# Performance work log

Measured on AMD Instinct MI355X. Metric: run time of the kernel, lower is better.

Reference implementation:

```python
import jax, jax.numpy as jnp
import numpy as np

SIGMA = 0.1
B = 1.0
SPATIAL_WEIGHT = 0.5
EPS = 1e-5


def setup_inputs() -> dict:
    key = jax.random.key(0)
    k1, k2 = jax.random.split(key)
    N, C, H, W = 2, 256, 64, 64
    I_features = jax.random.normal(k1, (N, C, H, W), dtype=jnp.float32)
    T_features = jax.random.normal(k2, (N, C, H, W), dtype=jnp.float32)
    return {"I_features": I_features, "T_features": T_features}


def _calc_cx(raw):
    # raw: [N, P_T, H, W]; min + exp-softmax over the target-patch axis (axis=1)
    mn = jnp.min(raw, axis=1, keepdims=True)
    rel = raw / (mn + EPS)
    w = jnp.exp((B - rel) / SIGMA)
    return w / jnp.sum(w, axis=1, keepdims=True)


def reference(I_features, T_features):
    N, C, H, W = I_features.shape
    P = H * W

    # ---- spatial branch: L2 distances on a normalized meshgrid (C=2) ----
    rows = jnp.arange(H, dtype=jnp.float32) / (H + 1)
    cols = jnp.arange(W, dtype=jnp.float32) / (W + 1)
    grid = jnp.stack(jnp.meshgrid(rows, cols, indexing="ij"))  # [2, H, W]
    g = grid.reshape(2, P)                                      # [2, P]
    sq = jnp.sum(g * g, axis=0)                                 # [P]
    d = sq[:, None] + sq[None, :] - 2.0 * (g.T @ g)             # [P_I, P_T]
    d = jnp.clip(d, 0.0)
    raw_sp = d.T.reshape(1, P, H, W)  # [1, P_T, H, W]; identical per sample
    cx_sp = _calc_cx(raw_sp)

    # ---- feature branch: cosine similarity via centered, L2-normed feats ----
    meanT = jnp.mean(T_features, axis=(0, 2, 3), keepdims=True)
    Ic = I_features - meanT
    Tc = T_features - meanT
    In = Ic / jnp.linalg.norm(Ic, axis=1, keepdims=True)
    Tn = Tc / jnp.linalg.norm(Tc, axis=1, keepdims=True)
    Iv = In.reshape(N, C, P)
    Tv = Tn.reshape(N, C, P)
    dot = jnp.einsum("ncq,ncp->nqp", Tv, Iv)  # [N, P_T, P_I]
    raw_feat = ((1.0 - dot) / 2.0).reshape(N, P, H, W)
    cx_feat = _calc_cx(raw_feat)

    # ---- combine, max over I positions, mean over T patches, -log, mean ----
    cx = (1.0 - SPATIAL_WEIGHT) * cx_feat + SPATIAL_WEIGHT * cx_sp  # [N,P,H,W]
    m = jnp.max(cx, axis=(2, 3))  # [N, P]
    m = jnp.mean(m, axis=1)       # [N]
    return jnp.mean(-jnp.log(m))
```

## Files before the change

kernel.cpp:

```cpp
#include <hip/hip_runtime.h>
#include <math.h>

#define PP 4096
#define CC 256
#define NN 2
#define NSTEP 16

typedef __attribute__((ext_vector_type(4))) float f32x4;
typedef __attribute__((ext_vector_type(8))) int i32x8;
typedef __attribute__((ext_vector_type(2))) int i32x2;


__global__ __launch_bounds__(256) void mean_kernel(const float* __restrict__ T,
                                                   float* __restrict__ meanT,
                                                   float* __restrict__ loss_acc) {
    int c = blockIdx.x, tid = threadIdx.x;
    float s = 0.f;
    for (int n = 0; n < NN; n++) {
        const float4* Tc = (const float4*)&T[(size_t)(n * CC + c) * PP];
        for (int g = 0; g < 4; g++) {
            float4 v = Tc[tid + g * 256];
            s += (v.x + v.y) + (v.z + v.w);
        }
    }
    __shared__ float red[256];
    red[tid] = s; __syncthreads();
    for (int st = 128; st > 0; st >>= 1) {
        if (tid < st) red[tid] += red[tid + st];
        __syncthreads();
    }
    if (tid == 0) meanT[c] = red[0] * (1.0f / (NN * PP));
    if (blockIdx.x == 0 && tid < NN) loss_acc[tid] = 0.f;
}

__global__ __launch_bounds__(256) void normalize_kernel(const float* __restrict__ I,
                                                        const float* __restrict__ T,
                                                        const float* __restrict__ meanT,
                                                        char* __restrict__ InT,
                                                        char* __restrict__ TnT) {
    int pc = blockIdx.x * 32;
    int n = blockIdx.y;
    int which = blockIdx.z;
    const float* X = which ? T : I;
    char* Y = (which ? TnT : InT) + (size_t)n * PP * CC;

    __shared__ float tile[CC][36];
    __shared__ float red[32][32];
    __shared__ float invn[32];

    int tid = threadIdx.x;
    int pl4 = tid & 7, c0 = tid >> 3;
    float sq0 = 0.f, sq1 = 0.f, sq2 = 0.f, sq3 = 0.f;
    for (int c = c0; c < CC; c += 32) {
        float m = meanT[c];
        float4 v = *(const float4*)&X[(size_t)(n * CC + c) * PP + pc + pl4 * 4];
        v.x -= m; v.y -= m; v.z -= m; v.w -= m;
        *(float4*)&tile[c][pl4 * 4] = v;
        sq0 += v.x * v.x; sq1 += v.y * v.y; sq2 += v.z * v.z; sq3 += v.w * v.w;
    }
    red[c0][pl4 * 4 + 0] = sq0;
    red[c0][pl4 * 4 + 1] = sq1;
    red[c0][pl4 * 4 + 2] = sq2;
    red[c0][pl4 * 4 + 3] = sq3;
    __syncthreads();
    if (tid < 32) {
        float s = 0.f;
        for (int k = 0; k < 32; k++) s += red[k][tid];
        invn[tid] = 1.0f / sqrtf(s);
    }
    __syncthreads();
    for (int pass = 0; pass < 8; pass++) {
        int r = pass * 4 + (tid >> 6);
        int p = pc + r;
        int c4 = (tid & 63) * 4;
        float in = invn[r];
        float v0 = tile[c4 + 0][r] * in;
        float v1 = tile[c4 + 1][r] * in;
        float v2 = tile[c4 + 2][r] * in;
        float v3 = tile[c4 + 3][r] * in;
        int w = __builtin_amdgcn_cvt_pk_fp8_f32(v0, v1, 0, false);
        w = __builtin_amdgcn_cvt_pk_fp8_f32(v2, v3, w, true);
        size_t addr = (size_t)(p >> 4) * 4096 + (c4 >> 5) * 512 +
                      ((c4 >> 3) & 3) * 128 + (p & 15) * 8 + (c4 & 7);
        *(unsigned*)&Y[addr] = (unsigned)w;
    }
}

__global__ __launch_bounds__(1024) void cx_strip(const char* __restrict__ TnT,
                                                 const char* __restrict__ InT,
                                                 float* __restrict__ loss_acc) {
    const int strip = blockIdx.x;
    const int n = blockIdx.y;
    const int p0 = strip * 32;
    const char* __restrict__ Ab = TnT + (size_t)n * PP * CC;
    const char* __restrict__ Bb = InT + (size_t)n * PP * CC;

    __shared__ float redw[16][32];
    __shared__ float inv2s[32];
    __shared__ float dwl[32];

    const int tid = threadIdx.x;
    const int l = tid & 63, wv = tid >> 6;
    const int lm = l & 15, quad = l >> 4;

    union BU { i32x2 d[2][8]; i32x8 v[2][2]; } bf;
#pragma unroll
    for (int ct = 0; ct < 2; ct++)
#pragma unroll
        for (int g = 0; g < 8; g++)
            bf.d[ct][g] = *(const i32x2*)(Bb + (size_t)(strip * 2 + ct) * 4096 +
                                          g * 512 + l * 8);

    const char* Abase = Ab + (size_t)wv * 4096 + l * 8;
    union AU { i32x2 d[8]; i32x8 v[2]; };

    float amax[2] = {-3.4e38f, -3.4e38f};
    float hc[2] = {0.f, 0.f}, c0c[2] = {0.f, 0.f};
    float ss[2] = {0.f, 0.f};
    const int qdd0 = p0 >> 8, wdd0 = (p0 >> 4) & 15;
    const int qdd1 = (p0 + 16) >> 8, wdd1 = ((p0 + 16) >> 4) & 15;

#pragma unroll 1
    for (int pass = 0; pass < 2; pass++) {
        AU cur, nxt;
#pragma unroll
        for (int g = 0; g < 8; g++)
            cur.d[g] = *(const i32x2*)(Abase + g * 512);

#pragma unroll 2
        for (int qs = 0; qs < NSTEP; qs++) {
            if (qs < NSTEP - 1) {
#pragma unroll
                for (int g = 0; g < 8; g++)
                    nxt.d[g] = *(const i32x2*)(Abase +
                        (size_t)(qs + 1) * 65536 + g * 512);
            }

            f32x4 acc[2] = {};
#pragma unroll
            for (int kb = 0; kb < 2; kb++)
#pragma unroll
                for (int ct = 0; ct < 2; ct++)
                    acc[ct] = __builtin_amdgcn_mfma_scale_f32_16x16x128_f8f6f4(
                        cur.v[kb], bf.v[ct][kb], acc[ct],
                        0, 0,
                        0, 0x7f7f7f7f,
                        0, 0x7f7f7f7f);

            if (pass == 0) {
#pragma unroll
                for (int ct = 0; ct < 2; ct++)
#pragma unroll
                    for (int e = 0; e < 4; e++)
                        amax[ct] = fmaxf(amax[ct], acc[ct][e]);
            } else {
#pragma unroll
                for (int ct = 0; ct < 2; ct++) {
                    float s2 = 0.f;
#pragma unroll
                    for (int e = 0; e < 4; e++)
                        s2 += exp2f(fmaf(acc[ct][e], hc[ct], c0c[ct]));
                    ss[ct] += s2;
                }
                if (qs == qdd0 && wv == wdd0 && quad == (lm >> 2))
                    dwl[lm] = exp2f(fmaf(acc[0][lm & 3], hc[0], c0c[0]));
                if (qs == qdd1 && wv == wdd1 && quad == (lm >> 2))
                    dwl[16 + lm] = exp2f(fmaf(acc[1][lm & 3], hc[1], c0c[1]));
            }

            if (qs < NSTEP - 1) cur = nxt;
        }

        if (pass == 0) {
#pragma unroll
            for (int ct = 0; ct < 2; ct++) {
                amax[ct] = fmaxf(amax[ct], __shfl_xor(amax[ct], 16));
                amax[ct] = fmaxf(amax[ct], __shfl_xor(amax[ct], 32));
                if (quad == 0) redw[wv][ct * 16 + lm] = amax[ct];
            }
            __syncthreads();
            if (tid < 32) {
                float mx = redw[0][tid];
#pragma unroll
                for (int w2 = 1; w2 < 16; w2++) mx = fmaxf(mx, redw[w2][tid]);
                float mnv = (1.0f - mx) * 0.5f;
                inv2s[tid] = 14.4269504f / (mnv + 1e-5f);
            }
            __syncthreads();
            {
                float i20 = inv2s[lm], i21 = inv2s[16 + lm];
                hc[0] = i20 * 0.5f; c0c[0] = 14.4269504f - hc[0];
                hc[1] = i21 * 0.5f; c0c[1] = 14.4269504f - hc[1];
            }
        }
    }

#pragma unroll
    for (int ct = 0; ct < 2; ct++) {
        ss[ct] += __shfl_xor(ss[ct], 16);
        ss[ct] += __shfl_xor(ss[ct], 32);
        if (quad == 0) redw[wv][ct * 16 + lm] = ss[ct];
    }
    __syncthreads();
    if (tid < 32) {
        float s = 0.f;
#pragma unroll
        for (int w2 = 0; w2 < 16; w2++) s += redw[w2][tid];
        float part = dwl[tid] / s;
        part += __shfl_xor(part, 1);
        part += __shfl_xor(part, 2);
        part += __shfl_xor(part, 4);
        part += __shfl_xor(part, 8);
        part += __shfl_xor(part, 16);
        if (tid == 0) atomicAdd(&loss_acc[n], part);
    }
}

__global__ void finalize_kernel(const float* __restrict__ loss_acc,
                                float* __restrict__ out) {
    float m0 = 0.5f + 0.5f * (loss_acc[0] / (float)PP);
    float m1 = 0.5f + 0.5f * (loss_acc[1] / (float)PP);
    out[0] = 0.5f * (-logf(m0) - logf(m1));
}

extern "C" void kernel_launch(void* const* d_in, const int* in_sizes, int n_in,
                              void* d_out, int out_size, void* d_ws, size_t ws_size,
                              hipStream_t stream) {
    const float* I = (const float*)d_in[0];
    const float* T = (const float*)d_in[1];
    float* out = (float*)d_out;

    char* ws = (char*)d_ws;
    const size_t SZ_F8 = (size_t)NN * PP * CC;
    char* InT = ws;
    char* TnT = ws + SZ_F8;
    float* meanT = (float*)(ws + 2 * SZ_F8);
    float* loss_acc = (float*)(ws + 2 * SZ_F8 + 32768);

    mean_kernel<<<CC, 256, 0, stream>>>(T, meanT, loss_acc);
    normalize_kernel<<<dim3(PP / 32, NN, 2), 256, 0, stream>>>(I, T, meanT, InT, TnT);
    cx_strip<<<dim3(PP / 32, NN), 1024, 0, stream>>>(TnT, InT, loss_acc);
    finalize_kernel<<<1, 1, 0, stream>>>(loss_acc, out);
}
```

Measured before the change: 110.0 us.

## Cache dot products in fp16 registers to drop second MFMA pass; stage A via LDS

The two-pass loop that recomputed the full FP8 MFMA GEMM (max pass, then exp-sum pass) becomes a single pass that keeps every dot product in registers as packed fp16 and then applies the exp-softmax sum from that cache. A tiles are now double-buffered through LDS with global_load_lds and explicit vmcnt waits instead of direct register loads. This halves GEMM work and global A traffic per strip, at the cost of 32 extra VGPRs per lane, 128KB of LDS per block, and fp16 rounding of the dot values before the exp.

```diff
diff --git a/kernel.cpp b/kernel.cpp
--- a/kernel.cpp
+++ b/kernel.cpp
@@ -9,6 +9,13 @@
 typedef __attribute__((ext_vector_type(4))) float f32x4;
 typedef __attribute__((ext_vector_type(8))) int i32x8;
 typedef __attribute__((ext_vector_type(2))) int i32x2;
+typedef _Float16 f16x2 __attribute__((ext_vector_type(2)));
+
+__device__ __forceinline__ void gld_lds16(const char* g, char* l) {
+    __builtin_amdgcn_global_load_lds(
+        (const __attribute__((address_space(1))) unsigned int*)g,
+        (__attribute__((address_space(3))) unsigned int*)l, 16, 0, 0);
+}
 
 
 __global__ __launch_bounds__(256) void mean_kernel(const float* __restrict__ T,
@@ -95,6 +102,7 @@
     const char* __restrict__ Ab = TnT + (size_t)n * PP * CC;
     const char* __restrict__ Bb = InT + (size_t)n * PP * CC;
 
+    __shared__ __align__(16) char Aw[16][2][4096];
     __shared__ float redw[16][32];
     __shared__ float inv2s[32];
     __shared__ float dwl[32];
@@ -111,87 +119,107 @@
             bf.d[ct][g] = *(const i32x2*)(Bb + (size_t)(strip * 2 + ct) * 4096 +
                                           g * 512 + l * 8);
 
-    const char* Abase = Ab + (size_t)wv * 4096 + l * 8;
-    union AU { i32x2 d[8]; i32x8 v[2]; };
-
+#define STAGE_A(qs, b)                                                        \
+    {                                                                         \
+        const char* s_ = Ab + (size_t)((qs) * 16 + wv) * 4096 + l * 16;       \
+        char* d_ = &Aw[wv][b][0] + l * 16;                                    \
+        _Pragma("unroll")                                                     \
+        for (int g_ = 0; g_ < 4; g_++)                                        \
+            gld_lds16(s_ + g_ * 1024, d_ + g_ * 1024);                        \
+    }
+
+    f16x2 dots[NSTEP][4];
     float amax[2] = {-3.4e38f, -3.4e38f};
-    float hc[2] = {0.f, 0.f}, c0c[2] = {0.f, 0.f};
-    float ss[2] = {0.f, 0.f};
     const int qdd0 = p0 >> 8, wdd0 = (p0 >> 4) & 15;
     const int qdd1 = (p0 + 16) >> 8, wdd1 = ((p0 + 16) >> 4) & 15;
 
-#pragma unroll 1
-    for (int pass = 0; pass < 2; pass++) {
-        AU cur, nxt;
+    STAGE_A(0, 0);
+#pragma unroll
+    for (int qs = 0; qs < NSTEP; qs++) {
+        if (qs < NSTEP - 1) {
+            STAGE_A(qs + 1, (qs + 1) & 1);
+            asm volatile("s_waitcnt vmcnt(4)" ::: "memory");
+        } else {
+            asm volatile("s_waitcnt vmcnt(0)" ::: "memory");
+        }
+        __builtin_amdgcn_sched_barrier(0);
+
+        const char* Ac = &Aw[wv][qs & 1][0];
+        union AU { long l2[8]; i32x8 v[2]; } a;
 #pragma unroll
         for (int g = 0; g < 8; g++)
-            cur.d[g] = *(const i32x2*)(Abase + g * 512);
-
-#pragma unroll 2
-        for (int qs = 0; qs < NSTEP; qs++) {
-            if (qs < NSTEP - 1) {
-#pragma unroll
-                for (int g = 0; g < 8; g++)
-                    nxt.d[g] = *(const i32x2*)(Abase +
-                        (size_t)(qs + 1) * 65536 + g * 512);
+            a.l2[g] = *(const long*)&Ac[g * 512 + l * 8];
+
+        f32x4 acc[2] = {};
+#pragma unroll
+        for (int kb = 0; kb < 2; kb++)
+#pragma unroll
+            for (int ct = 0; ct < 2; ct++)
+                acc[ct] = __builtin_amdgcn_mfma_scale_f32_16x16x128_f8f6f4(
+                    a.v[kb], bf.v[ct][kb], acc[ct],
+                    0, 0,
+                    0, 0x7f7f7f7f,
+                    0, 0x7f7f7f7f);
+
+#pragma unroll
+        for (int ct = 0; ct < 2; ct++) {
+#pragma unroll
+            for (int eh = 0; eh < 2; eh++) {
+                f16x2 t;
+                t.x = (_Float16)acc[ct][2 * eh];
+                t.y = (_Float16)acc[ct][2 * eh + 1];
+                dots[qs][ct * 2 + eh] = t;
             }
-
-            f32x4 acc[2] = {};
-#pragma unroll
-            for (int kb = 0; kb < 2; kb++)
-#pragma unroll
-                for (int ct = 0; ct < 2; ct++)
-                    acc[ct] = __builtin_amdgcn_mfma_scale_f32_16x16x128_f8f6f4(
-                        cur.v[kb], bf.v[ct][kb], acc[ct],
-                        0, 0,
-                        0, 0x7f7f7f7f,
-                        0, 0x7f7f7f7f);
-
-            if (pass == 0) {
-#pragma unroll
-                for (int ct = 0; ct < 2; ct++)
-#pragma unroll
-                    for (int e = 0; e < 4; e++)
-                        amax[ct] = fmaxf(amax[ct], acc[ct][e]);
-            } else {
-#pragma unroll
-                for (int ct = 0; ct < 2; ct++) {
-                    float s2 = 0.f;
-#pragma unroll
-                    for (int e = 0; e < 4; e++)
-                        s2 += exp2f(fmaf(acc[ct][e], hc[ct], c0c[ct]));
-                    ss[ct] += s2;
-                }
-                if (qs == qdd0 && wv == wdd0 && quad == (lm >> 2))
-                    dwl[lm] = exp2f(fmaf(acc[0][lm & 3], hc[0], c0c[0]));
-                if (qs == qdd1 && wv == wdd1 && quad == (lm >> 2))
-                    dwl[16 + lm] = exp2f(fmaf(acc[1][lm & 3], hc[1], c0c[1]));
-            }
-
-            if (qs < NSTEP - 1) cur = nxt;
-        }
-
-        if (pass == 0) {
-#pragma unroll
-            for (int ct = 0; ct < 2; ct++) {
-                amax[ct] = fmaxf(amax[ct], __shfl_xor(amax[ct], 16));
-                amax[ct] = fmaxf(amax[ct], __shfl_xor(amax[ct], 32));
-                if (quad == 0) redw[wv][ct * 16 + lm] = amax[ct];
-            }
-            __syncthreads();
-            if (tid < 32) {
-                float mx = redw[0][tid];
-#pragma unroll
-                for (int w2 = 1; w2 < 16; w2++) mx = fmaxf(mx, redw[w2][tid]);
-                float mnv = (1.0f - mx) * 0.5f;
-                inv2s[tid] = 14.4269504f / (mnv + 1e-5f);
-            }
-            __syncthreads();
-            {
-                float i20 = inv2s[lm], i21 = inv2s[16 + lm];
-                hc[0] = i20 * 0.5f; c0c[0] = 14.4269504f - hc[0];
-                hc[1] = i21 * 0.5f; c0c[1] = 14.4269504f - hc[1];
-            }
+#pragma unroll
+            for (int e = 0; e < 4; e++)
+                amax[ct] = fmaxf(amax[ct], acc[ct][e]);
+        }
+    }
+
+    float hc[2], c0c[2];
+#pragma unroll
+    for (int ct = 0; ct < 2; ct++) {
+        amax[ct] = fmaxf(amax[ct], __shfl_xor(amax[ct], 16));
+        amax[ct] = fmaxf(amax[ct], __shfl_xor(amax[ct], 32));
+        if (quad == 0) redw[wv][ct * 16 + lm] = amax[ct];
+    }
+    __syncthreads();
+    if (tid < 32) {
+        float mx = redw[0][tid];
+#pragma unroll
+        for (int w2 = 1; w2 < 16; w2++) mx = fmaxf(mx, redw[w2][tid]);
+        float mnv = (1.0f - mx) * 0.5f;
+        inv2s[tid] = 14.4269504f / (mnv + 1e-5f);
+    }
+    __syncthreads();
+    {
+        float i20 = inv2s[lm], i21 = inv2s[16 + lm];
+        hc[0] = i20 * 0.5f; c0c[0] = 14.4269504f - hc[0];
+        hc[1] = i21 * 0.5f; c0c[1] = 14.4269504f - hc[1];
+    }
+
+    float ss[2] = {0.f, 0.f};
+#pragma unroll
+    for (int qs = 0; qs < NSTEP; qs++) {
+#pragma unroll
+        for (int ct = 0; ct < 2; ct++) {
+            f16x2 d0 = dots[qs][ct * 2 + 0];
+            f16x2 d1 = dots[qs][ct * 2 + 1];
+            float w0 = exp2f(fmaf((float)d0.x, hc[ct], c0c[ct]));
+            float w1 = exp2f(fmaf((float)d0.y, hc[ct], c0c[ct]));
+            float w2 = exp2f(fmaf((float)d1.x, hc[ct], c0c[ct]));
+            float w3 = exp2f(fmaf((float)d1.y, hc[ct], c0c[ct]));
+            ss[ct] += (w0 + w1) + (w2 + w3);
+        }
+        if (qs == qdd0 && wv == wdd0 && quad == (lm >> 2)) {
+            f16x2 d = dots[qs][0 * 2 + ((lm >> 1) & 1)];
+            float dv = (lm & 1) ? (float)d.y : (float)d.x;
+            dwl[lm] = exp2f(fmaf(dv, hc[0], c0c[0]));
+        }
+        if (qs == qdd1 && wv == wdd1 && quad == (lm >> 2)) {
+            f16x2 d = dots[qs][1 * 2 + ((lm >> 1) & 1)];
+            float dv = (lm & 1) ? (float)d.y : (float)d.x;
+            dwl[16 + lm] = exp2f(fmaf(dv, hc[1], c0c[1]));
         }
     }
 
@@ -214,6 +242,7 @@
         part += __shfl_xor(part, 16);
         if (tid == 0) atomicAdd(&loss_acc[n], part);
     }
+#undef STAGE_A
 }
 
 __global__ void finalize_kernel(const float* __restrict__ loss_acc,
```

Measured after the change: 128.7 us. 1.17x slower.
